# Kernel optimization log

Hardware: AMD Instinct MI355X
Metric: run time of the kernel (lower is better)

Reference implementation:

```python
import jax, jax.numpy as jnp
import numpy as np
from jax import lax

B, C, H, W = 16, 64, 56, 56


def _conv2d(x, w, b, dilation, padding):
    y = lax.conv_general_dilated(
        x, w, window_strides=(1, 1),
        padding=((padding, padding), (padding, padding)),
        rhs_dilation=(dilation, dilation),
        dimension_numbers=('NCHW', 'OIHW', 'NCHW'))
    return y + b[None, :, None, None]


def setup_inputs() -> dict:
    key = jax.random.key(0)
    k1, k2, k3 = jax.random.split(key, 3)
    x = jax.random.normal(k1, (B, C, H, W), dtype=jnp.float32)
    w1 = jax.random.normal(k2, (128, C, 7, 7), dtype=jnp.float32) * 0.05
    b1 = jnp.zeros((128,), dtype=jnp.float32)
    w2 = jax.random.normal(k3, (49, 128, 1, 1), dtype=jnp.float32) * 0.05
    b2 = jnp.zeros((49,), dtype=jnp.float32)
    return {"x": x, "w1": w1, "b1": b1, "w2": w2, "b2": b2}


def reference(x, w1, b1, w2, b2):
    b_, c_, h_, w_ = x.shape
    # attention-kernel branch: conv(7x7, dil=2) -> 1x1 -> softmax over 49 channels
    k = _conv2d(x, w1, b1, dilation=2, padding=6)
    k = _conv2d(k, w2, b2, dilation=1, padding=0)
    attn = jax.nn.softmax(k, axis=1)  # [B, 49, H, W]

    # dilated 13x13 neighborhood sampled at stride-2 offsets -> 7x7 taps per pixel
    xp = jnp.pad(x, ((0, 0), (0, 0), (6, 6), (6, 6)))
    shifts = [xp[:, :, 2 * p:2 * p + h_, 2 * q:2 * q + w_]
              for p in range(7) for q in range(7)]
    patches = jnp.stack(shifts, axis=-1)  # [B, C, H, W, 49]

    # Faithful to torch .view/.reshape semantics (row-major): the original code
    # reshapes [B,C,H,W,kk] -> groups of size C and [B,49,H,W] -> [B*H*W,7,7]
    # WITHOUT permuting, so the group<->pixel correspondence is the row-major one.
    pg = patches.reshape(b_ * h_ * w_, c_, 49)  # == torch view(1,-1,C,13,13)[::2,::2]
    kg = attn.reshape(b_ * h_ * w_, 49)         # == torch reshape(B*H*W,1,1,7,7)
    out = jnp.einsum('gck,gk->gc', pg, kg)      # grouped conv3d, groups=B*H*W
    return out.reshape(b_, c_, h_, w_)
```

## Files before the change

### kernel.cpp

```cpp
#include <hip/hip_runtime.h>
#include <hip/hip_bf16.h>

#define HW 3136
#define NPIX 50176

typedef __attribute__((ext_vector_type(8))) _Float16 f16x8;
typedef __attribute__((ext_vector_type(4))) float f32x4;
typedef __attribute__((ext_vector_type(8))) unsigned short u16x8;

__device__ inline unsigned short f2h(float v){
    _Float16 h = (_Float16)v;
    union { _Float16 h; unsigned short u; } cv; cv.h = h; return cv.u;
}
__device__ inline float h2f(unsigned short u){
    union { unsigned short u; _Float16 h; } cv; cv.u = u; return (float)cv.h;
}

__global__ __launch_bounds__(256) void prep_all(
    const float* __restrict__ x, const float* __restrict__ w1,
    unsigned short* __restrict__ xg, unsigned short* __restrict__ w1t,
    unsigned short* __restrict__ xpad)
{
    int bb = blockIdx.x;
    if (bb < 392) {
        int t = bb * 256 + threadIdx.x;
        int g = t / NPIX;
        int pix = t - g * NPIX;
        int b = pix / HW; int s = pix - b * HW;
        const float* xp = x + (size_t)b * 64 * HW + (size_t)g * 32 * HW + s;
        unsigned short* dst = xg + ((size_t)(b * 2 + g) * HW + s) * 32;
#pragma unroll
        for (int p = 0; p < 4; ++p) {
            alignas(16) unsigned short tmp[8];
#pragma unroll
            for (int e = 0; e < 8; ++e)
                tmp[e] = f2h(xp[(size_t)(p * 8 + e) * HW]);
            *(u16x8*)(dst + p * 8) = *(const u16x8*)tmp;
        }
    } else if (bb < 664) {
        int t2 = (bb - 392) * 256 + threadIdx.x;
        int plane = t2 / 68; int r = t2 - plane * 68;
        unsigned short* dst = xpad + ((size_t)plane * 68 + r) * 72;
        int h = r - 6;
        alignas(16) unsigned short tmp[72];
#pragma unroll
        for (int i = 0; i < 72; ++i) tmp[i] = 0;
        if (h >= 0 && h < 56) {
            const float* src = x + (size_t)plane * HW + h * 56;
#pragma unroll
            for (int wq = 0; wq < 56; ++wq) tmp[6 + wq] = f2h(src[wq]);
        }
#pragma unroll
        for (int k = 0; k < 9; ++k)
            *(u16x8*)(dst + k * 8) = *(const u16x8*)(tmp + k * 8);
    } else {
        int t = (bb - 664) * 256 + threadIdx.x;
        if (t < 2 * 49 * 128) {
            int g = t / (49 * 128);
            int r = t - g * 49 * 128;
            int tap = r / 128; int oc = r - tap * 128;
            unsigned short* dst = w1t + (size_t)t * 32;
            for (int ic = 0; ic < 32; ++ic)
                dst[ic] = f2h(w1[((size_t)oc * 64 + g * 32 + ic) * 49 + tap]);
        }
    }
}

#define LOADA(Abuf, tap) do {                                                 \
    const int p_ = (tap) / 7, q_ = (tap) - 7 * ((tap) / 7);                   \
    const int off_ = p_ * 9792 + q_ * 144;                                    \
    _Pragma("unroll")                                                         \
    for (int mt = 0; mt < 7; ++mt)                                            \
        Abuf[mt] = *(const f16x8*)(smem + abase[mt] + off_);                  \
    } while (0)

#define LOADB(Bbuf, tap) do {                                                 \
    const unsigned short* p_ = wb + (size_t)(tap) * 4096;                     \
    Bbuf[0] = *(const f16x8*)(p_);                                            \
    Bbuf[1] = *(const f16x8*)(p_ + 512);                                      \
    Bbuf[2] = *(const f16x8*)(p_ + 1024);                                     \
    Bbuf[3] = *(const f16x8*)(p_ + 1536);                                     \
    } while (0)

#define DOMFMA(Abuf, Bbuf) do {                                               \
    __builtin_amdgcn_s_setprio(1);                                            \
    _Pragma("unroll")                                                         \
    for (int mt = 0; mt < 7; ++mt) {                                          \
        acc[mt][0] = __builtin_amdgcn_mfma_f32_16x16x32_f16(Abuf[mt], Bbuf[0], acc[mt][0], 0, 0, 0); \
        acc[mt][1] = __builtin_amdgcn_mfma_f32_16x16x32_f16(Abuf[mt], Bbuf[1], acc[mt][1], 0, 0, 0); \
        acc[mt][2] = __builtin_amdgcn_mfma_f32_16x16x32_f16(Abuf[mt], Bbuf[2], acc[mt][2], 0, 0, 0); \
        acc[mt][3] = __builtin_amdgcn_mfma_f32_16x16x32_f16(Abuf[mt], Bbuf[3], acc[mt][3], 0, 0, 0); \
    }                                                                         \
    __builtin_amdgcn_s_setprio(0);                                            \
    } while (0)

__global__ __launch_bounds__(256, 2) void conv_fused(
    const unsigned short* __restrict__ xg, const unsigned short* __restrict__ w1t,
    const float* __restrict__ b1, const float* __restrict__ w2,
    unsigned short* __restrict__ Lg0, unsigned short* __restrict__ Lg1)
{
    __shared__ char smem[78336];
    unsigned short* k1s = (unsigned short*)smem;
    unsigned short* w2s = (unsigned short*)(smem + 60928);

    const int blk = blockIdx.x;
    const int b   = blk / 28; int rem = blk - b * 28;
    const int g   = rem / 14; const int rg = rem - g * 14;
    const int h0  = rg * 4;
    const int tid = threadIdx.x;
    const int lane = tid & 63, warp = tid >> 6;
    const int wm  = warp >> 1, wn = warp & 1;
    const int oc0 = wn * 64;
    const int li  = lane & 15, j = lane >> 4;

    const unsigned short* xplane = xg + (size_t)(b * 2 + g) * HW * 32;
    u16x8 sv[14];
    u16x8 zz; for (int e = 0; e < 8; ++e) zz[e] = 0;
#pragma unroll
    for (int u = 0; u < 14; ++u) {
        int i = u * 256 + tid;
        int row = i / 224; int r2 = i - row * 224;
        int site = r2 >> 2, chunk = r2 & 3;
        int hh = h0 - 6 + row;
        sv[u] = (hh >= 0 && hh < 56)
            ? *(const u16x8*)(xplane + ((size_t)hh * 56 + site) * 32 + chunk * 8)
            : zz;
    }

    {
        f32x4 zv = {0.f, 0.f, 0.f, 0.f};
#pragma unroll 1
        for (int i = tid; i < 4896; i += 256)
            *(f32x4*)(smem + (size_t)i * 16) = zv;
    }
    __syncthreads();

#pragma unroll
    for (int u = 0; u < 14; ++u) {
        int i = u * 256 + tid;
        int row = i / 224; int r2 = i - row * 224;
        int site = r2 >> 2, chunk = r2 & 3;
        int hh = h0 - 6 + row;
        if (hh >= 0 && hh < 56)
            *(u16x8*)(smem + (row * 68 + 6 + site) * 72 + chunk * 16) = sv[u];
    }
    __syncthreads();

    int abase[7];
#pragma unroll
    for (int mt = 0; mt < 7; ++mt) {
        int local = wm * 112 + mt * 16 + li;
        int rb = local / 56; int wp = local - rb * 56;
        abase[mt] = (rb * 68 + wp) * 72 + j * 16;
    }

    f32x4 acc[7][4];
#pragma unroll
    for (int mt = 0; mt < 7; ++mt)
#pragma unroll
        for (int nt = 0; nt < 4; ++nt)
#pragma unroll
            for (int c = 0; c < 4; ++c) acc[mt][nt][c] = 0.f;

    const unsigned short* wb = w1t + ((size_t)g * 49 * 128 + oc0 + li) * 32 + j * 8;

    f16x8 A0[7], A1[7], B0[4], B1[4];
    LOADA(A0, 0); LOADB(B0, 0);
#pragma unroll
    for (int th = 0; th < 24; ++th) {
        LOADA(A1, 2 * th + 1); LOADB(B1, 2 * th + 1);
        __builtin_amdgcn_sched_barrier(0);
        DOMFMA(A0, B0);
        __builtin_amdgcn_sched_barrier(0);
        LOADA(A0, 2 * th + 2); LOADB(B0, 2 * th + 2);
        __builtin_amdgcn_sched_barrier(0);
        DOMFMA(A1, B1);
        __builtin_amdgcn_sched_barrier(0);
    }
    DOMFMA(A0, B0);

    f32x4 wv[7];
#pragma unroll
    for (int u = 0; u < 7; ++u) {
        int idx = u * 256 + tid;
        wv[u] = (idx < 1568) ? *(const f32x4*)(w2 + (size_t)idx * 4)
                             : (f32x4){0.f, 0.f, 0.f, 0.f};
    }
    __syncthreads();

    const int pixbase = wm * 112;
#pragma unroll
    for (int nt = 0; nt < 4; ++nt) {
        int oc = oc0 + nt * 16 + li;
        float bias = (g == 0) ? b1[oc] : 0.f;
#pragma unroll
        for (int mt = 0; mt < 7; ++mt) {
#pragma unroll
            for (int i = 0; i < 4; ++i) {
                int px = pixbase + mt * 16 + j * 4 + i;
                k1s[px * 136 + oc] = f2h(acc[mt][nt][i] + bias);
            }
        }
    }
#pragma unroll
    for (int u = 0; u < 7; ++u) {
        int idx = u * 256 + tid;
        if (idx < 1568) {
            int a = idx / 32; int c0 = (idx - a * 32) * 4;
            alignas(8) unsigned short t4[4];
#pragma unroll
            for (int e = 0; e < 4; ++e) t4[e] = f2h(wv[u][e]);
            *(unsigned long long*)(w2s + a * 136 + c0) = *(const unsigned long long*)t4;
        }
    }
    __syncthreads();

    const int start = (warp < 2) ? warp * 4 : 8 + (warp - 2) * 3;
    const int cnt   = (warp < 2) ? 4 : 3;
    unsigned short* Lg = (g == 0) ? Lg0 : Lg1;
    const size_t pxg0 = (size_t)b * HW + rg * 224;

#pragma unroll
    for (int u = 0; u < 4; ++u) {
        if (u < cnt) {
            int pxt = start + u;
            f32x4 a2[4];
#pragma unroll
            for (int tt = 0; tt < 4; ++tt)
#pragma unroll
                for (int c = 0; c < 4; ++c) a2[tt][c] = 0.f;
#pragma unroll
            for (int ks = 0; ks < 4; ++ks) {
                const f16x8 bf = *(const f16x8*)(k1s + (pxt * 16 + li) * 136 + ks * 32 + j * 8);
#pragma unroll
                for (int tt = 0; tt < 4; ++tt) {
                    const f16x8 af = *(const f16x8*)(w2s + (tt * 16 + li) * 136 + ks * 32 + j * 8);
                    a2[tt] = __builtin_amdgcn_mfma_f32_16x16x32_f16(af, bf, a2[tt], 0, 0, 0);
                }
            }
            size_t pxg = pxg0 + pxt * 16 + li;
#pragma unroll
            for (int tt = 0; tt < 4; ++tt)
#pragma unroll
                for (int i = 0; i < 4; ++i) {
                    int tap = tt * 16 + j * 4 + i;
                    if (tap < 49) Lg[pxg * 56 + tap] = f2h(a2[tt][i]);
                }
        }
    }
}

__global__ __launch_bounds__(256) void combine_softmax(
    const unsigned short* __restrict__ Lg0, const unsigned short* __restrict__ Lg1,
    const float* __restrict__ b2, unsigned short* __restrict__ attn)
{
    int px = blockIdx.x * 256 + threadIdx.x;
    int b = px / HW; int s = px - b * HW;
    const unsigned short* pa = Lg0 + (size_t)px * 56;
    const unsigned short* pb = Lg1 + (size_t)px * 56;
    float l[56];
#pragma unroll
    for (int c = 0; c < 7; ++c) {
        u16x8 va = *(const u16x8*)(pa + c * 8);
        u16x8 vb = *(const u16x8*)(pb + c * 8);
#pragma unroll
        for (int e = 0; e < 8; ++e) l[c * 8 + e] = h2f(va[e]) + h2f(vb[e]);
    }
    float mx = -3e38f;
#pragma unroll
    for (int a = 0; a < 49; ++a) { l[a] += b2[a]; mx = fmaxf(mx, l[a]); }
    float sum = 0.f;
#pragma unroll
    for (int a = 0; a < 49; ++a) { l[a] = __expf(l[a] - mx); sum += l[a]; }
    float inv = 1.f / sum;
    unsigned short* ap = attn + (size_t)b * 49 * HW + s;
#pragma unroll
    for (int a = 0; a < 49; ++a) ap[(size_t)a * HW] = f2h(l[a] * inv);
}

__global__ __launch_bounds__(256) void gather_kernel(
    const unsigned short* __restrict__ xpad, const unsigned short* __restrict__ attn,
    float* __restrict__ out)
{
    int tid = blockIdx.x * 256 + threadIdx.x;
    int plane = tid / 392;
    int r1 = tid - plane * 392;
    int h = r1 / 7; int oct = r1 - h * 7; int w0 = oct * 8;
    int F0 = plane * HW + h * 56 + w0;

    const unsigned short* ap = attn + (size_t)(F0 >> 6) * 49;
    float a[49];
#pragma unroll
    for (int k = 0; k < 49; ++k) a[k] = h2f(ap[k]);

    const unsigned short* xp = xpad + (size_t)plane * (68 * 72) + w0;
    float o[8];
#pragma unroll
    for (int dw = 0; dw < 8; ++dw) o[dw] = 0.f;

#pragma unroll
    for (int p = 0; p < 7; ++p) {
        const unsigned short* rp = xp + (h + 2 * p) * 72;
        u16x8 v0 = *(const u16x8*)rp;
        u16x8 v1 = *(const u16x8*)(rp + 8);
        u16x8 v2 = *(const u16x8*)(rp + 16);
        float rr[20];
#pragma unroll
        for (int e = 0; e < 8; ++e) { rr[e] = h2f(v0[e]); rr[8 + e] = h2f(v1[e]); }
#pragma unroll
        for (int e = 0; e < 4; ++e) rr[16 + e] = h2f(v2[e]);
#pragma unroll
        for (int q = 0; q < 7; ++q) {
            float aq = a[p * 7 + q];
#pragma unroll
            for (int dw = 0; dw < 8; ++dw)
                o[dw] = fmaf(rr[dw + 2 * q], aq, o[dw]);
        }
    }

    f32x4 s0 = {o[0], o[1], o[2], o[3]};
    f32x4 s1 = {o[4], o[5], o[6], o[7]};
    *(f32x4*)(out + F0) = s0;
    *(f32x4*)(out + F0 + 4) = s1;
}

extern "C" void kernel_launch(void* const* d_in, const int* in_sizes, int n_in,
                              void* d_out, int out_size, void* d_ws, size_t ws_size,
                              hipStream_t stream)
{
    const float* x  = (const float*)d_in[0];
    const float* w1 = (const float*)d_in[1];
    const float* b1 = (const float*)d_in[2];
    const float* w2 = (const float*)d_in[3];
    const float* b2 = (const float*)d_in[4];
    float* out = (float*)d_out;

    unsigned short* Lg0  = (unsigned short*)d_ws;
    unsigned short* Lg1  = Lg0 + (size_t)NPIX * 56;
    unsigned short* attn = Lg1 + (size_t)NPIX * 56;
    unsigned short* xg   = attn + (size_t)16 * 49 * HW;
    unsigned short* w1t  = xg + (size_t)16 * 2 * HW * 32;
    unsigned short* xpad = w1t + (size_t)2 * 49 * 128 * 32;

    prep_all<<<713, 256, 0, stream>>>(x, w1, xg, w1t, xpad);
    conv_fused<<<448, 256, 0, stream>>>(xg, w1t, b1, w2, Lg0, Lg1);
    combine_softmax<<<196, 256, 0, stream>>>(Lg0, Lg1, b2, attn);
    gather_kernel<<<1568, 256, 0, stream>>>(xpad, attn, out);
}
```

Baseline: 78.12 us.

## Fuse both channel-group convs and softmax into one 512-thread conv kernel

```diff
diff --git a/kernel.cpp b/kernel.cpp
--- a/kernel.cpp
+++ b/kernel.cpp
@@ -74,12 +74,10 @@
         Abuf[mt] = *(const f16x8*)(smem + abase[mt] + off_);                  \
     } while (0)
 
-#define LOADB(Bbuf, tap) do {                                                 \
-    const unsigned short* p_ = wb + (size_t)(tap) * 4096;                     \
+#define LOADB(Bbuf, wb, tap) do {                                             \
+    const unsigned short* p_ = (wb) + (size_t)(tap) * 4096;                   \
     Bbuf[0] = *(const f16x8*)(p_);                                            \
     Bbuf[1] = *(const f16x8*)(p_ + 512);                                      \
-    Bbuf[2] = *(const f16x8*)(p_ + 1024);                                     \
-    Bbuf[3] = *(const f16x8*)(p_ + 1536);                                     \
     } while (0)
 
 #define DOMFMA(Abuf, Bbuf) do {                                               \
@@ -88,61 +86,92 @@
     for (int mt = 0; mt < 7; ++mt) {                                          \
         acc[mt][0] = __builtin_amdgcn_mfma_f32_16x16x32_f16(Abuf[mt], Bbuf[0], acc[mt][0], 0, 0, 0); \
         acc[mt][1] = __builtin_amdgcn_mfma_f32_16x16x32_f16(Abuf[mt], Bbuf[1], acc[mt][1], 0, 0, 0); \
-        acc[mt][2] = __builtin_amdgcn_mfma_f32_16x16x32_f16(Abuf[mt], Bbuf[2], acc[mt][2], 0, 0, 0); \
-        acc[mt][3] = __builtin_amdgcn_mfma_f32_16x16x32_f16(Abuf[mt], Bbuf[3], acc[mt][3], 0, 0, 0); \
     }                                                                         \
     __builtin_amdgcn_s_setprio(0);                                            \
     } while (0)
 
-__global__ __launch_bounds__(256, 2) void conv_fused(
+#define TAPLOOP(wb) do {                                                      \
+    f16x8 A0[7], A1[7], B0[2], B1[2];                                         \
+    LOADA(A0, 0); LOADB(B0, wb, 0);                                           \
+    _Pragma("unroll")                                                         \
+    for (int th = 0; th < 24; ++th) {                                         \
+        LOADA(A1, 2 * th + 1); LOADB(B1, wb, 2 * th + 1);                     \
+        __builtin_amdgcn_sched_barrier(0);                                    \
+        DOMFMA(A0, B0);                                                       \
+        __builtin_amdgcn_sched_barrier(0);                                    \
+        LOADA(A0, 2 * th + 2); LOADB(B0, wb, 2 * th + 2);                     \
+        __builtin_amdgcn_sched_barrier(0);                                    \
+        DOMFMA(A1, B1);                                                       \
+        __builtin_amdgcn_sched_barrier(0);                                    \
+    }                                                                         \
+    DOMFMA(A0, B0);                                                           \
+    } while (0)
+
+__global__ __launch_bounds__(512, 2) void conv_full(
     const unsigned short* __restrict__ xg, const unsigned short* __restrict__ w1t,
     const float* __restrict__ b1, const float* __restrict__ w2,
-    unsigned short* __restrict__ Lg0, unsigned short* __restrict__ Lg1)
+    const float* __restrict__ b2, unsigned short* __restrict__ attn)
 {
     __shared__ char smem[78336];
     unsigned short* k1s = (unsigned short*)smem;
     unsigned short* w2s = (unsigned short*)(smem + 60928);
 
     const int blk = blockIdx.x;
-    const int b   = blk / 28; int rem = blk - b * 28;
-    const int g   = rem / 14; const int rg = rem - g * 14;
+    const int b   = blk / 14; const int rg = blk - b * 14;
     const int h0  = rg * 4;
     const int tid = threadIdx.x;
     const int lane = tid & 63, warp = tid >> 6;
-    const int wm  = warp >> 1, wn = warp & 1;
-    const int oc0 = wn * 64;
+    const int wm  = warp >> 2, wn = warp & 3;
+    const int oc0 = wn * 32;
     const int li  = lane & 15, j = lane >> 4;
 
-    const unsigned short* xplane = xg + (size_t)(b * 2 + g) * HW * 32;
-    u16x8 sv[14];
+    const unsigned short* xplane0 = xg + (size_t)(b * 2 + 0) * HW * 32;
+    const unsigned short* xplane1 = xg + (size_t)(b * 2 + 1) * HW * 32;
+
     u16x8 zz; for (int e = 0; e < 8; ++e) zz[e] = 0;
-#pragma unroll
-    for (int u = 0; u < 14; ++u) {
-        int i = u * 256 + tid;
+
+    u16x8 sv0[7];
+#pragma unroll
+    for (int u = 0; u < 7; ++u) {
+        int i = u * 512 + tid;
         int row = i / 224; int r2 = i - row * 224;
         int site = r2 >> 2, chunk = r2 & 3;
         int hh = h0 - 6 + row;
-        sv[u] = (hh >= 0 && hh < 56)
-            ? *(const u16x8*)(xplane + ((size_t)hh * 56 + site) * 32 + chunk * 8)
+        sv0[u] = (hh >= 0 && hh < 56)
+            ? *(const u16x8*)(xplane0 + ((size_t)hh * 56 + site) * 32 + chunk * 8)
             : zz;
     }
 
     {
         f32x4 zv = {0.f, 0.f, 0.f, 0.f};
-#pragma unroll 1
-        for (int i = tid; i < 4896; i += 256)
-            *(f32x4*)(smem + (size_t)i * 16) = zv;
-    }
-    __syncthreads();
-
-#pragma unroll
-    for (int u = 0; u < 14; ++u) {
-        int i = u * 256 + tid;
+#pragma unroll
+        for (int u = 0; u < 10; ++u) {
+            int i = u * 512 + tid;
+            if (i < 4896) *(f32x4*)(smem + (size_t)i * 16) = zv;
+        }
+    }
+    __syncthreads();
+
+#pragma unroll
+    for (int u = 0; u < 7; ++u) {
+        int i = u * 512 + tid;
         int row = i / 224; int r2 = i - row * 224;
         int site = r2 >> 2, chunk = r2 & 3;
         int hh = h0 - 6 + row;
         if (hh >= 0 && hh < 56)
-            *(u16x8*)(smem + (row * 68 + 6 + site) * 72 + chunk * 16) = sv[u];
+            *(u16x8*)(smem + (row * 68 + 6 + site) * 72 + chunk * 16) = sv0[u];
+    }
+
+    u16x8 sv1[7];
+#pragma unroll
+    for (int u = 0; u < 7; ++u) {
+        int i = u * 512 + tid;
+        int row = i / 224; int r2 = i - row * 224;
+        int site = r2 >> 2, chunk = r2 & 3;
+        int hh = h0 - 6 + row;
+        sv1[u] = (hh >= 0 && hh < 56)
+            ? *(const u16x8*)(xplane1 + ((size_t)hh * 56 + site) * 32 + chunk * 8)
+            : zz;
     }
     __syncthreads();
 
@@ -154,45 +183,47 @@
         abase[mt] = (rb * 68 + wp) * 72 + j * 16;
     }
 
-    f32x4 acc[7][4];
+    f32x4 acc[7][2];
 #pragma unroll
     for (int mt = 0; mt < 7; ++mt)
 #pragma unroll
-        for (int nt = 0; nt < 4; ++nt)
+        for (int nt = 0; nt < 2; ++nt)
 #pragma unroll
             for (int c = 0; c < 4; ++c) acc[mt][nt][c] = 0.f;
 
-    const unsigned short* wb = w1t + ((size_t)g * 49 * 128 + oc0 + li) * 32 + j * 8;
-
-    f16x8 A0[7], A1[7], B0[4], B1[4];
-    LOADA(A0, 0); LOADB(B0, 0);
-#pragma unroll
-    for (int th = 0; th < 24; ++th) {
-        LOADA(A1, 2 * th + 1); LOADB(B1, 2 * th + 1);
-        __builtin_amdgcn_sched_barrier(0);
-        DOMFMA(A0, B0);
-        __builtin_amdgcn_sched_barrier(0);
-        LOADA(A0, 2 * th + 2); LOADB(B0, 2 * th + 2);
-        __builtin_amdgcn_sched_barrier(0);
-        DOMFMA(A1, B1);
-        __builtin_amdgcn_sched_barrier(0);
-    }
-    DOMFMA(A0, B0);
-
-    f32x4 wv[7];
+    const unsigned short* wb0 = w1t + ((size_t)0 * 49 * 128 + oc0 + li) * 32 + j * 8;
+    const unsigned short* wb1 = w1t + ((size_t)1 * 49 * 128 + oc0 + li) * 32 + j * 8;
+
+    TAPLOOP(wb0);
+
+    __syncthreads();
 #pragma unroll
     for (int u = 0; u < 7; ++u) {
-        int idx = u * 256 + tid;
+        int i = u * 512 + tid;
+        int row = i / 224; int r2 = i - row * 224;
+        int site = r2 >> 2, chunk = r2 & 3;
+        int hh = h0 - 6 + row;
+        if (hh >= 0 && hh < 56)
+            *(u16x8*)(smem + (row * 68 + 6 + site) * 72 + chunk * 16) = sv1[u];
+    }
+    f32x4 wv[4];
+#pragma unroll
+    for (int u = 0; u < 4; ++u) {
+        int idx = u * 512 + tid;
         wv[u] = (idx < 1568) ? *(const f32x4*)(w2 + (size_t)idx * 4)
                              : (f32x4){0.f, 0.f, 0.f, 0.f};
     }
     __syncthreads();
 
+    TAPLOOP(wb1);
+
+    __syncthreads();
+
     const int pixbase = wm * 112;
 #pragma unroll
-    for (int nt = 0; nt < 4; ++nt) {
+    for (int nt = 0; nt < 2; ++nt) {
         int oc = oc0 + nt * 16 + li;
-        float bias = (g == 0) ? b1[oc] : 0.f;
+        float bias = b1[oc];
 #pragma unroll
         for (int mt = 0; mt < 7; ++mt) {
 #pragma unroll
@@ -203,8 +234,8 @@
         }
     }
 #pragma unroll
-    for (int u = 0; u < 7; ++u) {
-        int idx = u * 256 + tid;
+    for (int u = 0; u < 4; ++u) {
+        int idx = u * 512 + tid;
         if (idx < 1568) {
             int a = idx / 32; int c0 = (idx - a * 32) * 4;
             alignas(8) unsigned short t4[4];
@@ -215,13 +246,12 @@
     }
     __syncthreads();
 
-    const int start = (warp < 2) ? warp * 4 : 8 + (warp - 2) * 3;
-    const int cnt   = (warp < 2) ? 4 : 3;
-    unsigned short* Lg = (g == 0) ? Lg0 : Lg1;
-    const size_t pxg0 = (size_t)b * HW + rg * 224;
-
-#pragma unroll
-    for (int u = 0; u < 4; ++u) {
+    const int start = (warp < 6) ? warp * 2 : 12 + (warp - 6);
+    const int cnt   = (warp < 6) ? 2 : 1;
+    unsigned short* ab = attn + (size_t)b * 49 * HW;
+
+#pragma unroll
+    for (int u = 0; u < 2; ++u) {
         if (u < cnt) {
             int pxt = start + u;
             f32x4 a2[4];
@@ -238,44 +268,41 @@
                     a2[tt] = __builtin_amdgcn_mfma_f32_16x16x32_f16(af, bf, a2[tt], 0, 0, 0);
                 }
             }
-            size_t pxg = pxg0 + pxt * 16 + li;
+            float mx = -3e38f;
 #pragma unroll
             for (int tt = 0; tt < 4; ++tt)
 #pragma unroll
                 for (int i = 0; i < 4; ++i) {
-                    int tap = tt * 16 + j * 4 + i;
-                    if (tap < 49) Lg[pxg * 56 + tap] = f2h(a2[tt][i]);
+                    int r = tt * 16 + j * 4 + i;
+                    float v = a2[tt][i] + ((r < 49) ? b2[r] : 0.f);
+                    a2[tt][i] = v;
+                    if (r < 49) mx = fmaxf(mx, v);
                 }
-        }
-    }
-}
-
-__global__ __launch_bounds__(256) void combine_softmax(
-    const unsigned short* __restrict__ Lg0, const unsigned short* __restrict__ Lg1,
-    const float* __restrict__ b2, unsigned short* __restrict__ attn)
-{
-    int px = blockIdx.x * 256 + threadIdx.x;
-    int b = px / HW; int s = px - b * HW;
-    const unsigned short* pa = Lg0 + (size_t)px * 56;
-    const unsigned short* pb = Lg1 + (size_t)px * 56;
-    float l[56];
-#pragma unroll
-    for (int c = 0; c < 7; ++c) {
-        u16x8 va = *(const u16x8*)(pa + c * 8);
-        u16x8 vb = *(const u16x8*)(pb + c * 8);
-#pragma unroll
-        for (int e = 0; e < 8; ++e) l[c * 8 + e] = h2f(va[e]) + h2f(vb[e]);
-    }
-    float mx = -3e38f;
-#pragma unroll
-    for (int a = 0; a < 49; ++a) { l[a] += b2[a]; mx = fmaxf(mx, l[a]); }
-    float sum = 0.f;
-#pragma unroll
-    for (int a = 0; a < 49; ++a) { l[a] = __expf(l[a] - mx); sum += l[a]; }
-    float inv = 1.f / sum;
-    unsigned short* ap = attn + (size_t)b * 49 * HW + s;
-#pragma unroll
-    for (int a = 0; a < 49; ++a) ap[(size_t)a * HW] = f2h(l[a] * inv);
+            mx = fmaxf(mx, __shfl_xor(mx, 16));
+            mx = fmaxf(mx, __shfl_xor(mx, 32));
+            float sum = 0.f; float ex[16];
+#pragma unroll
+            for (int tt = 0; tt < 4; ++tt)
+#pragma unroll
+                for (int i = 0; i < 4; ++i) {
+                    int r = tt * 16 + j * 4 + i;
+                    float e = (r < 49) ? __expf(a2[tt][i] - mx) : 0.f;
+                    ex[tt * 4 + i] = e; sum += e;
+                }
+            sum += __shfl_xor(sum, 16);
+            sum += __shfl_xor(sum, 32);
+            float inv = 1.f / sum;
+
+            int s = rg * 224 + pxt * 16 + li;
+#pragma unroll
+            for (int tt = 0; tt < 4; ++tt)
+#pragma unroll
+                for (int i = 0; i < 4; ++i) {
+                    int r = tt * 16 + j * 4 + i;
+                    if (r < 49) ab[(size_t)r * HW + s] = f2h(ex[tt * 4 + i] * inv);
+                }
+        }
+    }
 }
 
 __global__ __launch_bounds__(256) void gather_kernel(
@@ -335,15 +362,12 @@
     const float* b2 = (const float*)d_in[4];
     float* out = (float*)d_out;
 
-    unsigned short* Lg0  = (unsigned short*)d_ws;
-    unsigned short* Lg1  = Lg0 + (size_t)NPIX * 56;
-    unsigned short* attn = Lg1 + (size_t)NPIX * 56;
+    unsigned short* attn = (unsigned short*)d_ws;
     unsigned short* xg   = attn + (size_t)16 * 49 * HW;
     unsigned short* w1t  = xg + (size_t)16 * 2 * HW * 32;
     unsigned short* xpad = w1t + (size_t)2 * 49 * 128 * 32;
 
     prep_all<<<713, 256, 0, stream>>>(x, w1, xg, w1t, xpad);
-    conv_fused<<<448, 256, 0, stream>>>(xg, w1t, b1, w2, Lg0, Lg1);
-    combine_softmax<<<196, 256, 0, stream>>>(Lg0, Lg1, b2, attn);
+    conv_full<<<224, 512, 0, stream>>>(xg, w1t, b1, w2, b2, attn);
     gather_kernel<<<1568, 256, 0, stream>>>(xpad, attn, out);
 }
```

Result: faster. 72.82 us (-6.8%).

## Fuse both channel groups and softmax into a single conv kernel

Applied to the files above, without the earlier changes.

```diff
diff --git a/kernel.cpp b/kernel.cpp
--- a/kernel.cpp
+++ b/kernel.cpp
@@ -94,55 +94,72 @@
     __builtin_amdgcn_s_setprio(0);                                            \
     } while (0)
 
-__global__ __launch_bounds__(256, 2) void conv_fused(
+__global__ __launch_bounds__(512, 2) void conv_full(
     const unsigned short* __restrict__ xg, const unsigned short* __restrict__ w1t,
     const float* __restrict__ b1, const float* __restrict__ w2,
-    unsigned short* __restrict__ Lg0, unsigned short* __restrict__ Lg1)
+    const float* __restrict__ b2, unsigned short* __restrict__ attn)
 {
-    __shared__ char smem[78336];
-    unsigned short* k1s = (unsigned short*)smem;
-    unsigned short* w2s = (unsigned short*)(smem + 60928);
+    __shared__ char smem[156672];
+    unsigned short* k1sa = (unsigned short*)smem;
+    unsigned short* w2s  = (unsigned short*)(smem + 60928);
+    unsigned short* k1sb = (unsigned short*)(smem + 78336);
 
     const int blk = blockIdx.x;
-    const int b   = blk / 28; int rem = blk - b * 28;
-    const int g   = rem / 14; const int rg = rem - g * 14;
+    const int b   = blk / 14; const int rg = blk - b * 14;
     const int h0  = rg * 4;
     const int tid = threadIdx.x;
     const int lane = tid & 63, warp = tid >> 6;
-    const int wm  = warp >> 1, wn = warp & 1;
+    const int g   = warp >> 2;
+    const int wm  = (warp >> 1) & 1, wn = warp & 1;
     const int oc0 = wn * 64;
     const int li  = lane & 15, j = lane >> 4;
 
-    const unsigned short* xplane = xg + (size_t)(b * 2 + g) * HW * 32;
+    const unsigned short* xplane[2] = {
+        xg + (size_t)(b * 2 + 0) * HW * 32,
+        xg + (size_t)(b * 2 + 1) * HW * 32 };
+
+    u16x8 zz; for (int e = 0; e < 8; ++e) zz[e] = 0;
+
     u16x8 sv[14];
-    u16x8 zz; for (int e = 0; e < 8; ++e) zz[e] = 0;
 #pragma unroll
     for (int u = 0; u < 14; ++u) {
-        int i = u * 256 + tid;
-        int row = i / 224; int r2 = i - row * 224;
+        int i = u * 512 + tid;
+        int pl = i / 3584; int rem = i - pl * 3584;
+        int row = rem / 224; int r2 = rem - row * 224;
         int site = r2 >> 2, chunk = r2 & 3;
         int hh = h0 - 6 + row;
         sv[u] = (hh >= 0 && hh < 56)
-            ? *(const u16x8*)(xplane + ((size_t)hh * 56 + site) * 32 + chunk * 8)
+            ? *(const u16x8*)(xplane[pl] + ((size_t)hh * 56 + site) * 32 + chunk * 8)
             : zz;
     }
 
     {
         f32x4 zv = {0.f, 0.f, 0.f, 0.f};
-#pragma unroll 1
-        for (int i = tid; i < 4896; i += 256)
-            *(f32x4*)(smem + (size_t)i * 16) = zv;
+#pragma unroll
+        for (int u = 0; u < 20; ++u) {
+            int i = u * 512 + tid;
+            if (i < 9792) *(f32x4*)(smem + (size_t)i * 16) = zv;
+        }
     }
     __syncthreads();
 
 #pragma unroll
     for (int u = 0; u < 14; ++u) {
-        int i = u * 256 + tid;
-        int row = i / 224; int r2 = i - row * 224;
+        int i = u * 512 + tid;
+        int pl = i / 3584; int rem = i - pl * 3584;
+        int row = rem / 224; int r2 = rem - row * 224;
         int site = r2 >> 2, chunk = r2 & 3;
         int hh = h0 - 6 + row;
         if (hh >= 0 && hh < 56)
-            *(u16x8*)(smem + (row * 68 + 6 + site) * 72 + chunk * 16) = sv[u];
+            *(u16x8*)(smem + pl * 78336 + (row * 68 + 6 + site) * 72 + chunk * 16) = sv[u];
+    }
+
+    f32x4 wv[4];
+#pragma unroll
+    for (int u = 0; u < 4; ++u) {
+        int idx = u * 512 + tid;
+        wv[u] = (idx < 1568) ? *(const f32x4*)(w2 + (size_t)idx * 4)
+                             : (f32x4){0.f, 0.f, 0.f, 0.f};
     }
     __syncthreads();
 
@@ -151,7 +168,7 @@
     for (int mt = 0; mt < 7; ++mt) {
         int local = wm * 112 + mt * 16 + li;
         int rb = local / 56; int wp = local - rb * 56;
-        abase[mt] = (rb * 68 + wp) * 72 + j * 16;
+        abase[mt] = g * 78336 + (rb * 68 + wp) * 72 + j * 16;
     }
 
     f32x4 acc[7][4];
@@ -164,47 +181,45 @@
 
     const unsigned short* wb = w1t + ((size_t)g * 49 * 128 + oc0 + li) * 32 + j * 8;
 
-    f16x8 A0[7], A1[7], B0[4], B1[4];
-    LOADA(A0, 0); LOADB(B0, 0);
-#pragma unroll
-    for (int th = 0; th < 24; ++th) {
-        LOADA(A1, 2 * th + 1); LOADB(B1, 2 * th + 1);
-        __builtin_amdgcn_sched_barrier(0);
+    {
+        f16x8 A0[7], A1[7], B0[4], B1[4];
+        LOADA(A0, 0); LOADB(B0, 0);
+#pragma unroll
+        for (int th = 0; th < 24; ++th) {
+            LOADA(A1, 2 * th + 1); LOADB(B1, 2 * th + 1);
+            __builtin_amdgcn_sched_barrier(0);
+            DOMFMA(A0, B0);
+            __builtin_amdgcn_sched_barrier(0);
+            LOADA(A0, 2 * th + 2); LOADB(B0, 2 * th + 2);
+            __builtin_amdgcn_sched_barrier(0);
+            DOMFMA(A1, B1);
+            __builtin_amdgcn_sched_barrier(0);
+        }
         DOMFMA(A0, B0);
-        __builtin_amdgcn_sched_barrier(0);
-        LOADA(A0, 2 * th + 2); LOADB(B0, 2 * th + 2);
-        __builtin_amdgcn_sched_barrier(0);
-        DOMFMA(A1, B1);
-        __builtin_amdgcn_sched_barrier(0);
-    }
-    DOMFMA(A0, B0);
-
-    f32x4 wv[7];
-#pragma unroll
-    for (int u = 0; u < 7; ++u) {
-        int idx = u * 256 + tid;
-        wv[u] = (idx < 1568) ? *(const f32x4*)(w2 + (size_t)idx * 4)
-                             : (f32x4){0.f, 0.f, 0.f, 0.f};
-    }
+    }
+
     __syncthreads();
 
-    const int pixbase = wm * 112;
-#pragma unroll
-    for (int nt = 0; nt < 4; ++nt) {
-        int oc = oc0 + nt * 16 + li;
-        float bias = (g == 0) ? b1[oc] : 0.f;
-#pragma unroll
-        for (int mt = 0; mt < 7; ++mt) {
-#pragma unroll
-            for (int i = 0; i < 4; ++i) {
-                int px = pixbase + mt * 16 + j * 4 + i;
-                k1s[px * 136 + oc] = f2h(acc[mt][nt][i] + bias);
+    {
+        unsigned short* kb = g ? k1sb : k1sa;
+        const int pixbase = wm * 112;
+#pragma unroll
+        for (int nt = 0; nt < 4; ++nt) {
+            int oc = oc0 + nt * 16 + li;
+            float bias = g ? 0.f : b1[oc];
+#pragma unroll
+            for (int mt = 0; mt < 7; ++mt) {
+#pragma unroll
+                for (int i = 0; i < 4; ++i) {
+                    int px = pixbase + mt * 16 + j * 4 + i;
+                    kb[px * 136 + oc] = f2h(acc[mt][nt][i] + bias);
+                }
             }
         }
     }
 #pragma unroll
-    for (int u = 0; u < 7; ++u) {
-        int idx = u * 256 + tid;
+    for (int u = 0; u < 4; ++u) {
+        int idx = u * 512 + tid;
         if (idx < 1568) {
             int a = idx / 32; int c0 = (idx - a * 32) * 4;
             alignas(8) unsigned short t4[4];
@@ -215,13 +230,12 @@
     }
     __syncthreads();
 
-    const int start = (warp < 2) ? warp * 4 : 8 + (warp - 2) * 3;
-    const int cnt   = (warp < 2) ? 4 : 3;
-    unsigned short* Lg = (g == 0) ? Lg0 : Lg1;
-    const size_t pxg0 = (size_t)b * HW + rg * 224;
-
-#pragma unroll
-    for (int u = 0; u < 4; ++u) {
+    const int start = (warp < 6) ? warp * 2 : 12 + (warp - 6);
+    const int cnt   = (warp < 6) ? 2 : 1;
+    unsigned short* ab = attn + (size_t)b * 49 * HW;
+
+#pragma unroll
+    for (int u = 0; u < 2; ++u) {
         if (u < cnt) {
             int pxt = start + u;
             f32x4 a2[4];
@@ -231,51 +245,50 @@
                 for (int c = 0; c < 4; ++c) a2[tt][c] = 0.f;
 #pragma unroll
             for (int ks = 0; ks < 4; ++ks) {
-                const f16x8 bf = *(const f16x8*)(k1s + (pxt * 16 + li) * 136 + ks * 32 + j * 8);
+                const f16x8 ba = *(const f16x8*)(k1sa + (pxt * 16 + li) * 136 + ks * 32 + j * 8);
+                const f16x8 bbv = *(const f16x8*)(k1sb + (pxt * 16 + li) * 136 + ks * 32 + j * 8);
+                const f16x8 bf = ba + bbv;
 #pragma unroll
                 for (int tt = 0; tt < 4; ++tt) {
                     const f16x8 af = *(const f16x8*)(w2s + (tt * 16 + li) * 136 + ks * 32 + j * 8);
                     a2[tt] = __builtin_amdgcn_mfma_f32_16x16x32_f16(af, bf, a2[tt], 0, 0, 0);
                 }
             }
-            size_t pxg = pxg0 + pxt * 16 + li;
+            float mx = -3e38f;
 #pragma unroll
             for (int tt = 0; tt < 4; ++tt)
 #pragma unroll
                 for (int i = 0; i < 4; ++i) {
-                    int tap = tt * 16 + j * 4 + i;
-                    if (tap < 49) Lg[pxg * 56 + tap] = f2h(a2[tt][i]);
-                }
-        }
-    }
-}
-
-__global__ __launch_bounds__(256) void combine_softmax(
-    const unsigned short* __restrict__ Lg0, const unsigned short* __restrict__ Lg1,
-    const float* __restrict__ b2, unsigned short* __restrict__ attn)
-{
-    int px = blockIdx.x * 256 + threadIdx.x;
-    int b = px / HW; int s = px - b * HW;
-    const unsigned short* pa = Lg0 + (size_t)px * 56;
-    const unsigned short* pb = Lg1 + (size_t)px * 56;
-    float l[56];
-#pragma unroll
-    for (int c = 0; c < 7; ++c) {
-        u16x8 va = *(const u16x8*)(pa + c * 8);
-        u16x8 vb = *(const u16x8*)(pb + c * 8);
-#pragma unroll
-        for (int e = 0; e < 8; ++e) l[c * 8 + e] = h2f(va[e]) + h2f(vb[e]);
-    }
-    float mx = -3e38f;
-#pragma unroll
-    for (int a = 0; a < 49; ++a) { l[a] += b2[a]; mx = fmaxf(mx, l[a]); }
-    float sum = 0.f;
-#pragma unroll
-    for (int a = 0; a < 49; ++a) { l[a] = __expf(l[a] - mx); sum += l[a]; }
-    float inv = 1.f / sum;
-    unsigned short* ap = attn + (size_t)b * 49 * HW + s;
-#pragma unroll
-    for (int a = 0; a < 49; ++a) ap[(size_t)a * HW] = f2h(l[a] * inv);
+                    int r = tt * 16 + j * 4 + i;
+                    float v = a2[tt][i] + ((r < 49) ? b2[r] : 0.f);
+                    a2[tt][i] = v;
+                    if (r < 49) mx = fmaxf(mx, v);
+                }
+            mx = fmaxf(mx, __shfl_xor(mx, 16));
+            mx = fmaxf(mx, __shfl_xor(mx, 32));
+            float sum = 0.f; float ex[16];
+#pragma unroll
+            for (int tt = 0; tt < 4; ++tt)
+#pragma unroll
+                for (int i = 0; i < 4; ++i) {
+                    int r = tt * 16 + j * 4 + i;
+                    float e = (r < 49) ? __expf(a2[tt][i] - mx) : 0.f;
+                    ex[tt * 4 + i] = e; sum += e;
+                }
+            sum += __shfl_xor(sum, 16);
+            sum += __shfl_xor(sum, 32);
+            float inv = 1.f / sum;
+
+            int s = rg * 224 + pxt * 16 + li;
+#pragma unroll
+            for (int tt = 0; tt < 4; ++tt)
+#pragma unroll
+                for (int i = 0; i < 4; ++i) {
+                    int r = tt * 16 + j * 4 + i;
+                    if (r < 49) ab[(size_t)r * HW + s] = f2h(ex[tt * 4 + i] * inv);
+                }
+        }
+    }
 }
 
 __global__ __launch_bounds__(256) void gather_kernel(
@@ -335,15 +348,12 @@
     const float* b2 = (const float*)d_in[4];
     float* out = (float*)d_out;
 
-    unsigned short* Lg0  = (unsigned short*)d_ws;
-    unsigned short* Lg1  = Lg0 + (size_t)NPIX * 56;
-    unsigned short* attn = Lg1 + (size_t)NPIX * 56;
+    unsigned short* attn = (unsigned short*)d_ws;
     unsigned short* xg   = attn + (size_t)16 * 49 * HW;
     unsigned short* w1t  = xg + (size_t)16 * 2 * HW * 32;
     unsigned short* xpad = w1t + (size_t)2 * 49 * 128 * 32;
 
     prep_all<<<713, 256, 0, stream>>>(x, w1, xg, w1t, xpad);
-    conv_fused<<<448, 256, 0, stream>>>(xg, w1t, b1, w2, Lg0, Lg1);
-    combine_softmax<<<196, 256, 0, stream>>>(Lg0, Lg1, b2, attn);
+    conv_full<<<224, 512, 0, stream>>>(xg, w1t, b1, w2, b2, attn);
     gather_kernel<<<1568, 256, 0, stream>>>(xpad, attn, out);
 }
```

Measured after the change: 72.43 us. -7.3%, faster.
